# Kernel tuning notes

Measured on AMD Instinct MI355X. Metric: run time of the kernel, lower is better.

The kernel has to match this reference:

```python
import jax, jax.numpy as jnp
import numpy as np
from jax import lax

DIM = 128
K = 3
PAD = K // 2


def setup_inputs() -> dict:
    key = jax.random.key(0)
    k1, k2, k3, k4, k5 = jax.random.split(key, 5)
    B, H, W = 64, 32, 32
    wdim = DIM * DIM * K * K + DIM  # 147584
    # scale question_rep (it encodes conv weights) for numerical sanity
    question_rep = jax.random.normal(k1, (B, wdim), dtype=jnp.float32) * 0.05
    lhs_rep = jax.random.normal(k2, (B, DIM, H, W), dtype=jnp.float32)
    rhs_rep = jax.random.normal(k3, (B, DIM, H, W), dtype=jnp.float32)
    proj_w = jax.random.normal(k4, (DIM, 2 * DIM), dtype=jnp.float32) * (1.0 / np.sqrt(2 * DIM))
    proj_b = jax.random.normal(k5, (DIM,), dtype=jnp.float32) * 0.01
    return {"question_rep": question_rep, "lhs_rep": lhs_rep,
            "rhs_rep": rhs_rep, "proj_w": proj_w, "proj_b": proj_b}


def _per_sample_conv(x, w, b):
    # x: [dim, H, W], w: [dim, dim, K, K], b: [dim]
    y = lax.conv_general_dilated(
        x[None], w, window_strides=(1, 1),
        padding=[(PAD, PAD), (PAD, PAD)],
        dimension_numbers=("NCHW", "OIHW", "NCHW"))
    return y[0] + b[:, None, None]


def reference(question_rep, lhs_rep, rhs_rep, proj_w, proj_b):
    B = question_rep.shape[0]
    wdim = DIM * DIM * K * K
    cnn_weight = question_rep[:, :wdim].reshape(B, DIM, DIM, K, K)
    cnn_bias = question_rep[:, wdim:]  # [B, dim]
    # 1x1 projection conv: cat along channels then contract
    cat = jnp.concatenate([lhs_rep, rhs_rep], axis=1)  # [B, 2*dim, H, W]
    cnn_inp = jnp.einsum("bchw,oc->bohw", cat, proj_w) + proj_b[None, :, None, None]
    # per-sample dynamic conv, vectorized over batch (equiv. grouped conv)
    out = jax.vmap(_per_sample_conv)(cnn_inp, cnn_weight, cnn_bias)
    return out
```

## Files before the change

kernel.cpp:

```cpp
#include <hip/hip_runtime.h>
#include <hip/hip_bf16.h>

#define QSTRIDE 147584
#define WOFF    147456

typedef __attribute__((ext_vector_type(8))) short bf16x8;
typedef __attribute__((ext_vector_type(4))) float f32x4;

static __device__ __forceinline__ ushort f2bf(float f) {
  union { float f; unsigned u; } x; x.f = f;
  unsigned r = x.u + 0x7fffu + ((x.u >> 16) & 1u);
  return (ushort)(r >> 16);
}
static __device__ __forceinline__ unsigned pk2(ushort a, ushort b) {
  return (unsigned)a | ((unsigned)b << 16);
}

__global__ __launch_bounds__(256) void prep_kernel(const float* __restrict__ q,
                                                   const float* __restrict__ pw,
                                                   const float* __restrict__ lhs,
                                                   const float* __restrict__ rhs,
                                                   ushort* __restrict__ wt2,
                                                   ushort* __restrict__ pwb2,
                                                   ushort* __restrict__ xt) {
  __shared__ __attribute__((aligned(16))) char smem[55296];
  int blk = blockIdx.x;
  int t = threadIdx.x;

  if (blk < 1024) {
    ushort (*Ts)[132] = (ushort(*)[132])smem;
    int b = blk >> 4, x = blk & 15;
    int c = x & 7, half = x >> 3;
    const float* src = (c < 4 ? lhs : rhs) + (size_t)b * 131072 + (size_t)(c & 3) * 32768;
    ushort* dst = xt + (size_t)(b * 8 + c) * 32768;
    int chw = t >> 3, pxg = (t & 7) * 16;
    int pxr = t >> 1, chr = (t & 1) * 16;
#pragma unroll
    for (int pt = 0; pt < 4; ++pt) {
      int p0 = half * 512 + pt * 128;
      if (pt) __syncthreads();
      const float* s = src + (size_t)chw * 1024 + p0 + pxg;
#pragma unroll
      for (int i = 0; i < 4; ++i) {
        float4 f = *(const float4*)(s + 4 * i);
        uint2 pk;
        pk.x = pk2(f2bf(f.x), f2bf(f.y));
        pk.y = pk2(f2bf(f.z), f2bf(f.w));
        *(uint2*)&Ts[chw][pxg + 4 * i] = pk;
      }
      __syncthreads();
      ushort g[16];
#pragma unroll
      for (int j = 0; j < 16; ++j) g[j] = Ts[chr + j][pxr];
      *(uint4*)(dst + (size_t)(p0 + pxr) * 32 + chr)     = *(uint4*)&g[0];
      *(uint4*)(dst + (size_t)(p0 + pxr) * 32 + chr + 8) = *(uint4*)&g[8];
    }
  } else if (blk < 1536) {
    float*  Ls = (float*)smem;
    ushort* Lw = (ushort*)(smem + 18432);
    int idx = blk - 1024;
    int b = idx >> 3, ogrp = idx & 7;
    const float* gbase = q + (size_t)b * QSTRIDE + (size_t)ogrp * 16 * 1152;
    int o_loc = t >> 6;
    int ci    = (t & 63) * 2;
    int cq    = ci >> 5, coff = ci & 31;
    for (int r = 0; r < 4; ++r) {
      __syncthreads();
      const float4* gs4 = (const float4*)(gbase + r * 4608);
      float4* Ls4 = (float4*)Ls;
#pragma unroll
      for (int i = 0; i < 4; ++i) Ls4[i * 256 + t] = gs4[i * 256 + t];
      if (t < 128) Ls4[1024 + t] = gs4[1024 + t];
      __syncthreads();
      int o_in = r * 4 + o_loc;
      const float* v = Ls + o_loc * 1152 + ci * 9;
      float a[18];
#pragma unroll
      for (int i = 0; i < 18; ++i) a[i] = v[i];
#pragma unroll
      for (int tap = 0; tap < 9; ++tap) {
        unsigned pkv = pk2(f2bf(a[tap]), f2bf(a[9 + tap]));
        *(unsigned*)&Lw[((tap * 4 + cq) * 16 + o_in) * 32 + coff] = pkv;
      }
    }
    __syncthreads();
    int wv = t >> 6, l = t & 63;
    ushort* dstb = wt2 + (size_t)b * 147456 + (size_t)ogrp * 16 * 32;
#pragma unroll
    for (int tap = 0; tap < 9; ++tap) {
      const uint4 val = *(const uint4*)&Lw[(tap * 4 + wv) * 512 + l * 8];
      *(uint4*)(dstb + (size_t)(tap * 4 + wv) * 4096 + l * 8) = val;
    }
  } else {
    int tg = (blk - 1536) * 256 + t;
    int o  = tg >> 5;
    int c0 = (tg & 31) * 8;
    const float4* s4 = (const float4*)(pw + (size_t)o * 256 + c0);
    float4 f0 = s4[0], f1 = s4[1];
    uint4 pkv;
    pkv.x = pk2(f2bf(f0.x), f2bf(f0.y)); pkv.y = pk2(f2bf(f0.z), f2bf(f0.w));
    pkv.z = pk2(f2bf(f1.x), f2bf(f1.y)); pkv.w = pk2(f2bf(f1.z), f2bf(f1.w));
    *(uint4*)(pwb2 + (size_t)(c0 >> 5) * 4096 + o * 32 + (c0 & 31)) = pkv;
  }
}

__global__ __launch_bounds__(256, 2) void fused_conv_kernel(const ushort* __restrict__ wt2,
                                                            const ushort* __restrict__ pwb2,
                                                            const ushort* __restrict__ xt,
                                                            const float* __restrict__ pb,
                                                            const float* __restrict__ q,
                                                            float* __restrict__ out) {
  __shared__ ushort Bs[4][6][34][32];
  int blk = blockIdx.x;
  int b = blk & 63, tile = blk >> 6;
  int p0 = tile * 128, h0 = tile * 4;
  int t = threadIdx.x;
  int lane = t & 63, wv = t >> 6;
  int quad = lane >> 4, li = lane & 15;

  if (t < 48) {
    int cq = t & 3, side = (t >> 2) & 1, rr = t >> 3;
    uint4* z4 = (uint4*)&Bs[cq][rr][side ? 33 : 0][0];
    uint4 z; z.x = z.y = z.z = z.w = 0u;
    z4[0] = z; z4[1] = z; z4[2] = z; z4[3] = z;
  }

  {
    int rk[3], wk[3], hk[3]; bool lv[3];
#pragma unroll
    for (int k = 0; k < 3; ++k) {
      int nt = wv * 3 + k;
      rk[k] = nt >> 1;
      wk[k] = (nt & 1) * 16;
      hk[k] = h0 - 1 + rk[k];
      lv[k] = (hk[k] >= 0) && (hk[k] < 32);
    }
    const ushort* xtb = xt + (size_t)b * 8 * 32768;
    f32x4 acc[3][8] = {};
#pragma unroll
    for (int c = 0; c < 8; ++c) {
      bf16x8 bg[3];
#pragma unroll
      for (int k = 0; k < 3; ++k) {
        union { uint4 u; bf16x8 v; } bu;
        if (lv[k]) {
          int px = hk[k] * 32 + wk[k] + li;
          bu.u = *(const uint4*)(xtb + ((size_t)c * 1024 + px) * 32 + quad * 8);
        } else {
          bu.u.x = bu.u.y = bu.u.z = bu.u.w = 0u;
        }
        bg[k] = bu.v;
      }
      const ushort* ap = pwb2 + (size_t)c * 4096 + li * 32 + quad * 8;
#pragma unroll
      for (int mi = 0; mi < 8; ++mi) {
        bf16x8 af = *(const bf16x8*)(ap + mi * 512);
#pragma unroll
        for (int k = 0; k < 3; ++k)
          acc[k][mi] = __builtin_amdgcn_mfma_f32_16x16x32_bf16(af, bg[k], acc[k][mi], 0, 0, 0);
      }
    }
#pragma unroll
    for (int k = 0; k < 3; ++k) {
#pragma unroll
      for (int mi = 0; mi < 8; ++mi) {
        int o0 = mi * 16 + quad * 4;
        uint2 pkv;
        if (lv[k]) {
          float4 bias = *(const float4*)(pb + o0);
          f32x4 a = acc[k][mi];
          pkv.x = pk2(f2bf(a.x + bias.x), f2bf(a.y + bias.y));
          pkv.y = pk2(f2bf(a.z + bias.z), f2bf(a.w + bias.w));
        } else {
          pkv.x = 0u; pkv.y = 0u;
        }
        *(uint2*)&Bs[o0 >> 5][rk[k]][wk[k] + li + 1][o0 & 31] = pkv;
      }
    }
  }
  __syncthreads();

  int m0 = (wv & 1) * 64, n0 = (wv >> 1) * 64;
  f32x4 acc2[4][4] = {};
  const ushort* wtb = wt2 + (size_t)b * 147456;
#pragma unroll
  for (int cq = 0; cq < 4; ++cq) {
    const ushort* wcq = wtb + (size_t)cq * 4096;
#pragma unroll
    for (int tap = 0; tap < 9; ++tap) {
      const ushort* ar = wcq + (size_t)tap * 16384;
      int kh = tap / 3, kw = tap - kh * 3;
      bf16x8 af[4], bg[4];
#pragma unroll
      for (int mi = 0; mi < 4; ++mi)
        af[mi] = *(const bf16x8*)(ar + (m0 + mi*16 + li) * 32 + quad * 8);
#pragma unroll
      for (int ni = 0; ni < 4; ++ni) {
        int pl = n0 + ni*16 + li;
        int hh = pl >> 5, ww = pl & 31;
        bg[ni] = *(const bf16x8*)&Bs[cq][hh + kh][ww + kw][quad * 8];
      }
#pragma unroll
      for (int mi = 0; mi < 4; ++mi)
#pragma unroll
        for (int ni = 0; ni < 4; ++ni)
          acc2[mi][ni] = __builtin_amdgcn_mfma_f32_16x16x32_bf16(af[mi], bg[ni], acc2[mi][ni], 0, 0, 0);
    }
  }

  const float* qb = q + (size_t)b * QSTRIDE + WOFF;
  float* ob = out + (size_t)b * 128 * 1024 + p0;
#pragma unroll
  for (int mi = 0; mi < 4; ++mi) {
    int o0 = m0 + mi*16 + quad*4;
    float4 bias = *(const float4*)(qb + o0);
#pragma unroll
    for (int ni = 0; ni < 4; ++ni) {
      int pl = n0 + ni*16 + li;
      float* dp = ob + (size_t)o0 * 1024 + pl;
      f32x4 a = acc2[mi][ni];
      dp[0]    = a.x + bias.x;
      dp[1024] = a.y + bias.y;
      dp[2048] = a.z + bias.z;
      dp[3072] = a.w + bias.w;
    }
  }
}

extern "C" void kernel_launch(void* const* d_in, const int* in_sizes, int n_in,
                              void* d_out, int out_size, void* d_ws, size_t ws_size,
                              hipStream_t stream) {
  const float* q   = (const float*)d_in[0];
  const float* lhs = (const float*)d_in[1];
  const float* rhs = (const float*)d_in[2];
  const float* pw  = (const float*)d_in[3];
  const float* pb  = (const float*)d_in[4];
  float* out = (float*)d_out;

  char* ws = (char*)d_ws;
  ushort* wt2  = (ushort*)(ws);
  ushort* pwb2 = (ushort*)(ws + 18874368);
  ushort* xt   = (ushort*)(ws + 18939904);

  prep_kernel      <<<1552, 256, 0, stream>>>(q, pw, lhs, rhs, wt2, pwb2, xt);
  fused_conv_kernel<<<512,  256, 0, stream>>>(wt2, pwb2, xt, pb, q, out);
}
```

Baseline: 182.4 us.

## Halve conv pixel tile to 2 rows and simplify weight-prep blocks

The fused conv kernel now processes 64 pixels (2 rows) per block instead of 128, doubling the grid to 1024 blocks and raising the occupancy hint to 4 blocks per CU with a smaller LDS halo buffer. The weight-prep path is rewritten so each block handles 8 output channels by loading directly from global memory into registers, dropping the float staging buffer in shared memory and cutting prep LDS use. The cost is more redundant 1x1 projection work on halo rows (4 rows computed per 2 output rows instead of 6 per 4) and more re-reads of per-sample weights across blocks.

```diff
diff --git a/kernel.cpp b/kernel.cpp
--- a/kernel.cpp
+++ b/kernel.cpp
@@ -23,7 +23,7 @@
                                                    ushort* __restrict__ wt2,
                                                    ushort* __restrict__ pwb2,
                                                    ushort* __restrict__ xt) {
-  __shared__ __attribute__((aligned(16))) char smem[55296];
+  __shared__ __attribute__((aligned(16))) char smem[18432];
   int blk = blockIdx.x;
   int t = threadIdx.x;
 
@@ -55,44 +55,36 @@
       *(uint4*)(dst + (size_t)(p0 + pxr) * 32 + chr)     = *(uint4*)&g[0];
       *(uint4*)(dst + (size_t)(p0 + pxr) * 32 + chr + 8) = *(uint4*)&g[8];
     }
-  } else if (blk < 1536) {
-    float*  Ls = (float*)smem;
-    ushort* Lw = (ushort*)(smem + 18432);
+  } else if (blk < 2048) {
+    ushort* Lw = (ushort*)smem;
     int idx = blk - 1024;
-    int b = idx >> 3, ogrp = idx & 7;
-    const float* gbase = q + (size_t)b * QSTRIDE + (size_t)ogrp * 16 * 1152;
-    int o_loc = t >> 6;
-    int ci    = (t & 63) * 2;
-    int cq    = ci >> 5, coff = ci & 31;
-    for (int r = 0; r < 4; ++r) {
-      __syncthreads();
-      const float4* gs4 = (const float4*)(gbase + r * 4608);
-      float4* Ls4 = (float4*)Ls;
-#pragma unroll
-      for (int i = 0; i < 4; ++i) Ls4[i * 256 + t] = gs4[i * 256 + t];
-      if (t < 128) Ls4[1024 + t] = gs4[1024 + t];
-      __syncthreads();
-      int o_in = r * 4 + o_loc;
-      const float* v = Ls + o_loc * 1152 + ci * 9;
-      float a[18];
-#pragma unroll
-      for (int i = 0; i < 18; ++i) a[i] = v[i];
-#pragma unroll
-      for (int tap = 0; tap < 9; ++tap) {
-        unsigned pkv = pk2(f2bf(a[tap]), f2bf(a[9 + tap]));
-        *(unsigned*)&Lw[((tap * 4 + cq) * 16 + o_in) * 32 + coff] = pkv;
-      }
+    int b = idx >> 4, og = idx & 15;
+    int o_loc = t >> 5, c4 = t & 31;
+    int ci0 = c4 * 4;
+    int cq = ci0 >> 5, coff = ci0 & 31;
+    const float4* src = (const float4*)(q + (size_t)b * QSTRIDE
+                          + (size_t)(og * 8 + o_loc) * 1152 + (size_t)ci0 * 9);
+    float4 ff[9];
+#pragma unroll
+    for (int i = 0; i < 9; ++i) ff[i] = src[i];
+    const float* v = (const float*)ff;
+#pragma unroll
+    for (int tap = 0; tap < 9; ++tap) {
+      uint2 pkv;
+      pkv.x = pk2(f2bf(v[tap]),      f2bf(v[9 + tap]));
+      pkv.y = pk2(f2bf(v[18 + tap]), f2bf(v[27 + tap]));
+      *(uint2*)&Lw[((tap * 4 + cq) * 8 + o_loc) * 32 + coff] = pkv;
     }
     __syncthreads();
     int wv = t >> 6, l = t & 63;
-    ushort* dstb = wt2 + (size_t)b * 147456 + (size_t)ogrp * 16 * 32;
+    ushort* dstb = wt2 + (size_t)b * 147456 + (size_t)og * 256;
 #pragma unroll
     for (int tap = 0; tap < 9; ++tap) {
-      const uint4 val = *(const uint4*)&Lw[(tap * 4 + wv) * 512 + l * 8];
-      *(uint4*)(dstb + (size_t)(tap * 4 + wv) * 4096 + l * 8) = val;
+      uint2 val = *(const uint2*)&Lw[(tap * 4 + wv) * 256 + l * 4];
+      *(uint2*)(dstb + (size_t)(tap * 4 + wv) * 4096 + l * 4) = val;
     }
   } else {
-    int tg = (blk - 1536) * 256 + t;
+    int tg = (blk - 2048) * 256 + t;
     int o  = tg >> 5;
     int c0 = (tg & 31) * 8;
     const float4* s4 = (const float4*)(pw + (size_t)o * 256 + c0);
@@ -104,21 +96,21 @@
   }
 }
 
-__global__ __launch_bounds__(256, 2) void fused_conv_kernel(const ushort* __restrict__ wt2,
+__global__ __launch_bounds__(256, 4) void fused_conv_kernel(const ushort* __restrict__ wt2,
                                                             const ushort* __restrict__ pwb2,
                                                             const ushort* __restrict__ xt,
                                                             const float* __restrict__ pb,
                                                             const float* __restrict__ q,
                                                             float* __restrict__ out) {
-  __shared__ ushort Bs[4][6][34][32];
+  __shared__ ushort Bs[4][4][34][32];
   int blk = blockIdx.x;
   int b = blk & 63, tile = blk >> 6;
-  int p0 = tile * 128, h0 = tile * 4;
+  int p0 = tile * 64, h0 = tile * 2;
   int t = threadIdx.x;
   int lane = t & 63, wv = t >> 6;
   int quad = lane >> 4, li = lane & 15;
 
-  if (t < 48) {
+  if (t < 32) {
     int cq = t & 3, side = (t >> 2) & 1, rr = t >> 3;
     uint4* z4 = (uint4*)&Bs[cq][rr][side ? 33 : 0][0];
     uint4 z; z.x = z.y = z.z = z.w = 0u;
@@ -126,25 +118,18 @@
   }
 
   {
-    int rk[3], wk[3], hk[3]; bool lv[3];
-#pragma unroll
-    for (int k = 0; k < 3; ++k) {
-      int nt = wv * 3 + k;
-      rk[k] = nt >> 1;
-      wk[k] = (nt & 1) * 16;
-      hk[k] = h0 - 1 + rk[k];
-      lv[k] = (hk[k] >= 0) && (hk[k] < 32);
-    }
+    int h = h0 - 1 + wv;
+    bool lv = (h >= 0) && (h < 32);
     const ushort* xtb = xt + (size_t)b * 8 * 32768;
-    f32x4 acc[3][8] = {};
+    f32x4 acc[2][8] = {};
 #pragma unroll
     for (int c = 0; c < 8; ++c) {
-      bf16x8 bg[3];
-#pragma unroll
-      for (int k = 0; k < 3; ++k) {
+      bf16x8 bg[2];
+#pragma unroll
+      for (int k = 0; k < 2; ++k) {
         union { uint4 u; bf16x8 v; } bu;
-        if (lv[k]) {
-          int px = hk[k] * 32 + wk[k] + li;
+        if (lv) {
+          int px = h * 32 + k * 16 + li;
           bu.u = *(const uint4*)(xtb + ((size_t)c * 1024 + px) * 32 + quad * 8);
         } else {
           bu.u.x = bu.u.y = bu.u.z = bu.u.w = 0u;
@@ -156,17 +141,17 @@
       for (int mi = 0; mi < 8; ++mi) {
         bf16x8 af = *(const bf16x8*)(ap + mi * 512);
 #pragma unroll
-        for (int k = 0; k < 3; ++k)
+        for (int k = 0; k < 2; ++k)
           acc[k][mi] = __builtin_amdgcn_mfma_f32_16x16x32_bf16(af, bg[k], acc[k][mi], 0, 0, 0);
       }
     }
 #pragma unroll
-    for (int k = 0; k < 3; ++k) {
+    for (int k = 0; k < 2; ++k) {
 #pragma unroll
       for (int mi = 0; mi < 8; ++mi) {
         int o0 = mi * 16 + quad * 4;
         uint2 pkv;
-        if (lv[k]) {
+        if (lv) {
           float4 bias = *(const float4*)(pb + o0);
           f32x4 a = acc[k][mi];
           pkv.x = pk2(f2bf(a.x + bias.x), f2bf(a.y + bias.y));
@@ -174,14 +159,14 @@
         } else {
           pkv.x = 0u; pkv.y = 0u;
         }
-        *(uint2*)&Bs[o0 >> 5][rk[k]][wk[k] + li + 1][o0 & 31] = pkv;
+        *(uint2*)&Bs[o0 >> 5][wv][k * 16 + li + 1][o0 & 31] = pkv;
       }
     }
   }
   __syncthreads();
 
-  int m0 = (wv & 1) * 64, n0 = (wv >> 1) * 64;
-  f32x4 acc2[4][4] = {};
+  int m0 = (wv & 1) * 64, n0 = (wv >> 1) * 32;
+  f32x4 acc2[4][2] = {};
   const ushort* wtb = wt2 + (size_t)b * 147456;
 #pragma unroll
   for (int cq = 0; cq < 4; ++cq) {
@@ -190,12 +175,12 @@
     for (int tap = 0; tap < 9; ++tap) {
       const ushort* ar = wcq + (size_t)tap * 16384;
       int kh = tap / 3, kw = tap - kh * 3;
-      bf16x8 af[4], bg[4];
+      bf16x8 af[4], bg[2];
 #pragma unroll
       for (int mi = 0; mi < 4; ++mi)
         af[mi] = *(const bf16x8*)(ar + (m0 + mi*16 + li) * 32 + quad * 8);
 #pragma unroll
-      for (int ni = 0; ni < 4; ++ni) {
+      for (int ni = 0; ni < 2; ++ni) {
         int pl = n0 + ni*16 + li;
         int hh = pl >> 5, ww = pl & 31;
         bg[ni] = *(const bf16x8*)&Bs[cq][hh + kh][ww + kw][quad * 8];
@@ -203,7 +188,7 @@
 #pragma unroll
       for (int mi = 0; mi < 4; ++mi)
 #pragma unroll
-        for (int ni = 0; ni < 4; ++ni)
+        for (int ni = 0; ni < 2; ++ni)
           acc2[mi][ni] = __builtin_amdgcn_mfma_f32_16x16x32_bf16(af[mi], bg[ni], acc2[mi][ni], 0, 0, 0);
     }
   }
@@ -215,7 +200,7 @@
     int o0 = m0 + mi*16 + quad*4;
     float4 bias = *(const float4*)(qb + o0);
 #pragma unroll
-    for (int ni = 0; ni < 4; ++ni) {
+    for (int ni = 0; ni < 2; ++ni) {
       int pl = n0 + ni*16 + li;
       float* dp = ob + (size_t)o0 * 1024 + pl;
       f32x4 a = acc2[mi][ni];
@@ -242,6 +227,6 @@
   ushort* pwb2 = (ushort*)(ws + 18874368);
   ushort* xt   = (ushort*)(ws + 18939904);
 
-  prep_kernel      <<<1552, 256, 0, stream>>>(q, pw, lhs, rhs, wt2, pwb2, xt);
-  fused_conv_kernel<<<512,  256, 0, stream>>>(wt2, pwb2, xt, pb, q, out);
-}
+  prep_kernel      <<<2064, 256, 0, stream>>>(q, pw, lhs, rhs, wt2, pwb2, xt);
+  fused_conv_kernel<<<1024, 256, 0, stream>>>(wt2, pwb2, xt, pb, q, out);
+}
```

Result: slower. 209.7 us (+15.0%).
